# Kernel tuning notes

Measured on AMD Instinct MI355X. Metric: run time of the kernel, lower is better.

Reference implementation:

```python
import jax, jax.numpy as jnp
import numpy as np

TOPK = 13
ALPHA = 1.0
BETA = 6.0
NUM_CLASSES = 80
NUM_ANCHORS = 100000
NUM_GT = 512
EPS = 1e-9


def _make_boxes(key, n):
    k1, k2 = jax.random.split(key)
    lt = jax.random.uniform(k1, (n, 2)) * 0.5          # x1, y1 in [0, 0.5)
    wh = jax.random.uniform(k2, (n, 2)) * 0.5 + 1e-3   # positive width/height
    return jnp.concatenate([lt, lt + wh], axis=-1)      # [n, 4] valid xyxy


def setup_inputs() -> dict:
    key = jax.random.key(0)
    k1, k2, k3, k4 = jax.random.split(key, 4)
    pd_scores = jax.random.uniform(k1, (NUM_ANCHORS, NUM_CLASSES), dtype=jnp.float32)
    pd_bboxes = _make_boxes(k2, NUM_ANCHORS)
    gt_labels = jax.random.randint(k3, (NUM_GT, 1), 0, NUM_CLASSES, dtype=jnp.int64)
    gt_bboxes = _make_boxes(k4, NUM_GT)
    return {"pd_scores": pd_scores, "pd_bboxes": pd_bboxes,
            "gt_labels": gt_labels, "gt_bboxes": gt_bboxes}


def box_iou(a, b):
    # a: [G, 4], b: [A, 4] in xyxy -> iou [G, A]
    lt = jnp.maximum(a[:, None, :2], b[None, :, :2])
    rb = jnp.minimum(a[:, None, 2:], b[None, :, 2:])
    wh = jnp.clip(rb - lt, 0.0)
    inter = wh[..., 0] * wh[..., 1]                      # [G, A]
    area_a = (a[:, 2] - a[:, 0]) * (a[:, 3] - a[:, 1])   # [G]
    area_b = (b[:, 2] - b[:, 0]) * (b[:, 3] - b[:, 1])   # [A]
    union = area_a[:, None] + area_b[None, :] - inter
    return inter / (union + EPS)


def select_topk_candidates(metrics, topk):
    # metrics: [G, A] -> bool mask [G, A] of per-row topk entries
    _, topk_idx = jax.lax.top_k(metrics, topk)           # [G, topk]
    rows = jnp.arange(metrics.shape[0])[:, None]
    mask = jnp.zeros(metrics.shape, dtype=bool)
    return mask.at[rows, topk_idx].set(True)


def reference(pd_scores, pd_bboxes, gt_labels, gt_bboxes):
    labels = gt_labels.reshape(-1)                       # [G]
    ious = box_iou(gt_bboxes, pd_bboxes)                 # [G, A]
    scores = pd_scores[:, labels].T                      # [G, A] gather by gt class
    metrics = (scores ** ALPHA) * (ious ** BETA)         # alignment metric [G, A]
    is_in_topk = select_topk_candidates(metrics, TOPK)   # [G, A] bool
    max_metrics = jnp.max(metrics, axis=0)               # [A]
    max_indices = jnp.argmax(metrics, axis=0)            # [A]
    target_labels = labels[max_indices]                  # [A]
    target_labels = jnp.where(max_metrics <= 0, NUM_CLASSES, target_labels)
    target_bboxes = gt_bboxes[max_indices]               # [A, 4]
    # is_in_topk is computed (as in the original) and returned so the topk/scatter
    return target_labels, target_bboxes, max_metrics, is_in_topk
```

## Files before the change

### kernel.cpp

```cpp
#include <hip/hip_runtime.h>
#include <cfloat>
#include <cstdint>

#define AN 100000
#define GN 512
#define NC 80
#define KK 13

#define CHUNKS 8
#define CH_LEN 12544
#define DUMP 16
#define GSLICE 8
#define GPS (GN / GSLICE)

typedef unsigned long long ull;

__device__ __forceinline__ float rcpf(float x)
{
    float r; asm("v_rcp_f32 %0, %1" : "=v"(r) : "v"(x)); return r;
}

__device__ __forceinline__ float root6_down(float th)
{
    return exp2f(log2f(th) * (1.0f / 6.0f)) * 0.9999f;
}

__device__ __forceinline__ float iou6r(float4 g, float ga, float4 p)
{
    float pa = (p.z - p.x) * (p.w - p.y);
    float ltx = fmaxf(g.x, p.x), lty = fmaxf(g.y, p.y);
    float rbx = fminf(g.z, p.z), rby = fminf(g.w, p.w);
    float w = fmaxf(rbx - ltx, 0.0f), h = fmaxf(rby - lty, 0.0f);
    float inter = w * h;
    float uni = ga + pa - inter;
    float iou = inter * rcpf(uni + 1e-9f);
    float i2 = iou * iou;
    return i2 * i2 * i2;
}

__device__ __forceinline__ unsigned f2ord(float f)
{
    unsigned b = __float_as_uint(f);
    return b ^ (unsigned)(((int)b >> 31) | 0x80000000);
}
__device__ __forceinline__ float ord2f(unsigned u)
{
    unsigned b = (u & 0x80000000u) ? (u ^ 0x80000000u) : ~u;
    return __uint_as_float(b);
}

__device__ __forceinline__ void csw(float& va, int& ia, float& vb, int& ib)
{
    bool sw = (va < vb) || (va == vb && ia > ib);
    float tv = sw ? vb : va; int ti = sw ? ib : ia;
    vb = sw ? va : vb; ib = sw ? ia : ib;
    va = tv; ia = ti;
}

__device__ __forceinline__ void wsync()
{
    __builtin_amdgcn_sched_barrier(0);
    asm volatile("s_waitcnt lgkmcnt(0)" ::: "memory");
    __builtin_amdgcn_sched_barrier(0);
}

__device__ float flush_f(int lane, int n,
                         const float* c_in, const float* c_ue, const int* c_ix,
                         const float* __restrict__ srow,
                         float& inc_v, int& inc_i)
{
    wsync();
    float v[8]; int ix[8];
    #pragma unroll
    for (int k = 0; k < 8; ++k) {
        int j = lane + (k << 6);
        bool ok = j < n;
        float in = ok ? c_in[j] : 0.0f;
        float ue = ok ? c_ue[j] : 1.0f;
        int   ai = ok ? c_ix[j] : 0;
        float iou = in * rcpf(ue);
        float i2 = iou * iou;
        float i6 = i2 * i2 * i2;
        float sc = srow[ai];
        v[k]  = ok ? sc * i6 : -FLT_MAX;
        ix[k] = ok ? ai : 0x7fffffff;
    }
    csw(v[0],ix[0],v[1],ix[1]); csw(v[2],ix[2],v[3],ix[3]);
    csw(v[4],ix[4],v[5],ix[5]); csw(v[6],ix[6],v[7],ix[7]);
    csw(v[0],ix[0],v[2],ix[2]); csw(v[1],ix[1],v[3],ix[3]);
    csw(v[4],ix[4],v[6],ix[6]); csw(v[5],ix[5],v[7],ix[7]);
    csw(v[1],ix[1],v[2],ix[2]); csw(v[5],ix[5],v[6],ix[6]);
    csw(v[0],ix[0],v[4],ix[4]); csw(v[1],ix[1],v[5],ix[5]);
    csw(v[2],ix[2],v[6],ix[6]); csw(v[3],ix[3],v[7],ix[7]);
    csw(v[2],ix[2],v[4],ix[4]); csw(v[3],ix[3],v[5],ix[5]);
    csw(v[1],ix[1],v[2],ix[2]); csw(v[3],ix[3],v[4],ix[4]);
    csw(v[5],ix[5],v[6],ix[6]);
    bool c[8];
    #pragma unroll
    for (int j = 0; j < 8; ++j)
        c[j] = (v[j] > inc_v) || (v[j] == inc_v && ix[j] < inc_i);
    float h[9]; int hi[9];
    h[0] = c[0] ? v[0] : inc_v;  hi[0] = c[0] ? ix[0] : inc_i;
    #pragma unroll
    for (int j = 1; j < 8; ++j) {
        h[j]  = c[j] ? v[j]  : (c[j-1] ? inc_v : v[j-1]);
        hi[j] = c[j] ? ix[j] : (c[j-1] ? inc_i : ix[j-1]);
    }
    h[8] = c[7] ? inc_v : v[7];  hi[8] = c[7] ? inc_i : ix[7];

    float th = -FLT_MAX;
    #pragma unroll
    for (int r = 0; r < KK; ++r) {
        ull myp = ((ull)f2ord(h[0]) << 32) | (unsigned)(~hi[0]);
        ull p = myp;
        #pragma unroll
        for (int o = 32; o >= 1; o >>= 1) {
            ull q = __shfl_xor(p, o);
            p = p > q ? p : q;
        }
        float wv = ord2f((unsigned)(p >> 32));
        int   wi = (int)~((unsigned)p);
        if (lane == r) { inc_v = wv; inc_i = wi; }
        bool pop = (myp == p);
        #pragma unroll
        for (int j = 0; j < 8; ++j) {
            h[j]  = pop ? h[j+1]  : h[j];
            hi[j] = pop ? hi[j+1] : hi[j];
        }
        h[8]  = pop ? -FLT_MAX   : h[8];
        hi[8] = pop ? 0x7fffffff : hi[8];
        th = wv;
    }
    return th;
}

__device__ __forceinline__ void insert13(float* v, int* ix, float m, int a)
{
    bool worse = (m < v[KK - 1]) || (m == v[KK - 1] && a > ix[KK - 1]);
    if (worse) return;
    int p = 0;
    #pragma unroll
    for (int j = 0; j < KK; ++j)
        p += ((v[j] > m) || (v[j] == m && ix[j] < a)) ? 1 : 0;
    #pragma unroll
    for (int j = KK - 1; j >= 1; --j) {
        bool sh = (j > p);
        v[j]  = sh ? v[j - 1]  : v[j];
        ix[j] = sh ? ix[j - 1] : ix[j];
    }
    #pragma unroll
    for (int j = 0; j < KK; ++j) if (j == p) { v[j] = m; ix[j] = a; }
}

__global__ __launch_bounds__(256) void transpose_scores(
    const float* __restrict__ ps, float* __restrict__ scT)
{
    __shared__ float tile[64][NC + 1];
    int a0 = blockIdx.x * 64;
    int tid = threadIdx.x;
    for (int i = tid; i < 64 * NC / 4; i += 256) {
        int fi = i * 4;
        int a = fi / NC, c = fi % NC;
        if (a0 + a < AN) {
            float4 v = *reinterpret_cast<const float4*>(ps + (size_t)(a0 + a) * NC + c);
            tile[a][c] = v.x; tile[a][c + 1] = v.y; tile[a][c + 2] = v.z; tile[a][c + 3] = v.w;
        }
    }
    __syncthreads();
    int j = tid & 63, cg = tid >> 6;
    int a = a0 + j;
    if (a < AN) {
        for (int c = cg; c < NC; c += 4)
            scT[(size_t)c * AN + a] = tile[j][c];
    }
}

__global__ __launch_bounds__(256) void argmax_part(
    const float* __restrict__ pd_bboxes,
    const int*   __restrict__ gt_labels,
    const float* __restrict__ gt_bboxes,
    const float* __restrict__ scT,
    ull* __restrict__ part)
{
    __shared__ float4 gb[GPS];
    __shared__ float  ga[GPS];
    __shared__ int    glb[GPS];
    int slice = blockIdx.x & (GSLICE - 1);
    int ab = (blockIdx.x >> 3) * 512;
    int tid = threadIdx.x;
    int g0 = slice * GPS;
    if (tid < GPS) {
        float4 bb = ((const float4*)gt_bboxes)[g0 + tid];
        gb[tid] = bb;
        ga[tid] = (bb.z - bb.x) * (bb.w - bb.y);
        glb[tid] = gt_labels[g0 + tid];
    }
    __syncthreads();
    int aa = ab + tid, ab2 = ab + 256 + tid;
    bool okA = aa < AN, okB = ab2 < AN;
    int ca = okA ? aa : AN - 1, cb = okB ? ab2 : AN - 1;
    float4 pba = ((const float4*)pd_bboxes)[ca];
    float4 pbb = ((const float4*)pd_bboxes)[cb];
    float bestA = -1.0f, bestB = -1.0f;
    int bgA = 0, bgB = 0;
    for (int i = 0; i < GPS; ++i) {
        float4 gx = gb[i];
        float gax = ga[i];
        int lab = glb[i];
        const float* srow = scT + (size_t)lab * AN;
        float i6a = iou6r(gx, gax, pba);
        float i6b = iou6r(gx, gax, pbb);
        float sa = (i6a > bestA) ? srow[ca] : 0.0f;
        float sb = (i6b > bestB) ? srow[cb] : 0.0f;
        float ma = sa * i6a;
        float mb = sb * i6b;
        if (ma > bestA) { bestA = ma; bgA = i; }
        if (mb > bestB) { bestB = mb; bgB = i; }
    }
    if (okA)
        part[(size_t)slice * AN + aa] =
            ((ull)__float_as_uint(bestA) << 32) | (ull)(0xFFFFFFFFu - (unsigned)(g0 + bgA));
    if (okB)
        part[(size_t)slice * AN + ab2] =
            ((ull)__float_as_uint(bestB) << 32) | (ull)(0xFFFFFFFFu - (unsigned)(g0 + bgB));
}

__global__ __launch_bounds__(256) void argmax_combine(
    const ull* __restrict__ part,
    const int* __restrict__ gt_labels,
    const float* __restrict__ gt_bboxes,
    float* __restrict__ out)
{
    int a = blockIdx.x * 256 + threadIdx.x;
    if (a >= AN) return;
    ull p = part[a];
    #pragma unroll
    for (int s = 1; s < GSLICE; ++s) {
        ull q = part[(size_t)s * AN + a];
        p = p > q ? p : q;
    }
    unsigned g = 0xFFFFFFFFu - (unsigned)(p & 0xFFFFFFFFull);
    float best = __uint_as_float((unsigned)(p >> 32));
    out[a] = (best <= 0.0f) ? (float)NC : (float)gt_labels[g];
    ((float4*)(out + AN))[a] = ((const float4*)gt_bboxes)[g];
    out[(size_t)5 * AN + a] = best;
}

__device__ __forceinline__ void loadB(int tb, int lane,
    const float4* __restrict__ pd4,
    float4& B0, float4& B1, float4& B2, float4& B3)
{
    int a0 = tb + lane;
    B0 = pd4[min(a0,       AN - 1)];
    B1 = pd4[min(a0 + 64,  AN - 1)];
    B2 = pd4[min(a0 + 128, AN - 1)];
    B3 = pd4[min(a0 + 192, AN - 1)];
}

__device__ __forceinline__ void procB(
    int tb, int aend, int lane, uint64_t lt,
    float4 B0, float4 B1, float4 B2, float4 B3,
    const float* __restrict__ srow,
    float4 b, float gax, float& th, float& cth, int& cnt,
    float* c_in, float* c_ue, int* c_ix,
    float& inc_v, int& inc_i)
{
    int a0 = tb + lane, a1 = a0 + 64, a2 = a0 + 128, a3 = a0 + 192;
    float lx0 = fmaxf(b.x, B0.x), ly0 = fmaxf(b.y, B0.y);
    float rx0 = fminf(b.z, B0.z), ry0 = fminf(b.w, B0.w);
    float w0 = fmaxf(rx0 - lx0, 0.0f), h0f = fmaxf(ry0 - ly0, 0.0f);
    float in0 = w0 * h0f;
    float ue0 = gax + (B0.z - B0.x) * (B0.w - B0.y) - in0 + 1e-9f;
    float lx1 = fmaxf(b.x, B1.x), ly1 = fmaxf(b.y, B1.y);
    float rx1 = fminf(b.z, B1.z), ry1 = fminf(b.w, B1.w);
    float w1 = fmaxf(rx1 - lx1, 0.0f), h1f = fmaxf(ry1 - ly1, 0.0f);
    float in1 = w1 * h1f;
    float ue1 = gax + (B1.z - B1.x) * (B1.w - B1.y) - in1 + 1e-9f;
    float lx2 = fmaxf(b.x, B2.x), ly2 = fmaxf(b.y, B2.y);
    float rx2 = fminf(b.z, B2.z), ry2 = fminf(b.w, B2.w);
    float w2 = fmaxf(rx2 - lx2, 0.0f), h2f = fmaxf(ry2 - ly2, 0.0f);
    float in2 = w2 * h2f;
    float ue2 = gax + (B2.z - B2.x) * (B2.w - B2.y) - in2 + 1e-9f;
    float lx3 = fmaxf(b.x, B3.x), ly3 = fmaxf(b.y, B3.y);
    float rx3 = fminf(b.z, B3.z), ry3 = fminf(b.w, B3.w);
    float w3 = fmaxf(rx3 - lx3, 0.0f), h3f = fmaxf(ry3 - ly3, 0.0f);
    float in3 = w3 * h3f;
    float ue3 = gax + (B3.z - B3.x) * (B3.w - B3.y) - in3 + 1e-9f;
    bool h0 = (in0 > cth * ue0) && (a0 < aend);
    bool h1 = (in1 > cth * ue1) && (a1 < aend);
    bool h2 = (in2 > cth * ue2) && (a2 < aend);
    bool h3 = (in3 > cth * ue3) && (a3 < aend);
    if (__any(h0 | h1 | h2 | h3)) {
        uint64_t B;
        B = __ballot(h0);
        if (h0) { int p = cnt + __popcll(B & lt); c_in[p] = in0; c_ue[p] = ue0; c_ix[p] = a0; }
        cnt += __popcll(B);
        B = __ballot(h1);
        if (h1) { int p = cnt + __popcll(B & lt); c_in[p] = in1; c_ue[p] = ue1; c_ix[p] = a1; }
        cnt += __popcll(B);
        B = __ballot(h2);
        if (h2) { int p = cnt + __popcll(B & lt); c_in[p] = in2; c_ue[p] = ue2; c_ix[p] = a2; }
        cnt += __popcll(B);
        B = __ballot(h3);
        if (h3) { int p = cnt + __popcll(B & lt); c_in[p] = in3; c_ue[p] = ue3; c_ix[p] = a3; }
        cnt += __popcll(B);
        if (cnt >= 256) {
            th = flush_f(lane, cnt, c_in, c_ue, c_ix, srow, inc_v, inc_i);
            cth = root6_down(th);
            cnt = 0;
        }
    }
}

__global__ __launch_bounds__(256, 4) void topk_pass1(
    const float* __restrict__ pd_bboxes,
    const int*   __restrict__ gt_labels,
    const float* __restrict__ gt_bboxes,
    const float* __restrict__ scT,
    float* __restrict__ out_v, int* __restrict__ out_i)
{
    __shared__ float cinA[4][512];
    __shared__ float cueA[4][512];
    __shared__ int   cixA[4][512];
    int w = threadIdx.x >> 6, lane = threadIdx.x & 63;
    float* c_in = cinA[w]; float* c_ue = cueA[w]; int* c_ix = cixA[w];
    uint64_t lt = (1ull << lane) - 1ull;
    int gid = blockIdx.x * 4 + w;
    int g = gid & (GN - 1), c = gid >> 9;

    float4 b = ((const float4*)gt_bboxes)[g];
    float gax = (b.z - b.x) * (b.w - b.y);
    int lab = gt_labels[g];
    const float* srow = scT + (size_t)lab * AN;
    const float4* pd4 = (const float4*)pd_bboxes;

    int base = c * CH_LEN;
    int len = min(CH_LEN, AN - base);
    int aend = base + len;
    int NT = (len + 255) >> 8;

    float th = -FLT_MAX, cth = -FLT_MAX;
    int cnt = 0;
    float inc_v = -FLT_MAX; int inc_i = 0x7fffffff;

    float4 X0, X1, X2, X3, Y0, Y1, Y2, Y3;
    loadB(base, lane, pd4, X0, X1, X2, X3);
    int i = 0, tb = base;
    while (true) {
        if (i + 1 < NT) loadB(tb + 256, lane, pd4, Y0, Y1, Y2, Y3);
        procB(tb, aend, lane, lt, X0, X1, X2, X3, srow,
              b, gax, th, cth, cnt, c_in, c_ue, c_ix, inc_v, inc_i);
        ++i; tb += 256;
        if (i >= NT) break;
        if (i + 1 < NT) loadB(tb + 256, lane, pd4, X0, X1, X2, X3);
        procB(tb, aend, lane, lt, Y0, Y1, Y2, Y3, srow,
              b, gax, th, cth, cnt, c_in, c_ue, c_ix, inc_v, inc_i);
        ++i; tb += 256;
        if (i >= NT) break;
    }

    if (cnt > 0)
        flush_f(lane, cnt, c_in, c_ue, c_ix, srow, inc_v, inc_i);

    if (lane < DUMP) {
        size_t o = ((size_t)g * CHUNKS + c) * DUMP + lane;
        out_v[o] = (lane < KK) ? inc_v : -FLT_MAX;
        out_i[o] = (lane < KK) ? inc_i : 0x7fffffff;
    }
}

__global__ __launch_bounds__(256) void topk_finalize(
    const float* __restrict__ in_v, const int* __restrict__ in_i,
    float* __restrict__ mask)
{
    int g = blockIdx.x, tid = threadIdx.x;
    float4* row4 = (float4*)(mask + (size_t)g * AN);
    float4 z = make_float4(0.f, 0.f, 0.f, 0.f);
    for (int j = tid; j < AN / 4; j += 256) row4[j] = z;
    __syncthreads();
    if (tid >= 64) return;
    int lane = tid;
    size_t rb = (size_t)g * (CHUNKS * DUMP);
    float v0 = in_v[rb + lane], v1 = in_v[rb + 64 + lane];
    int   i0 = in_i[rb + lane], i1 = in_i[rb + 64 + lane];
    csw(v0, i0, v1, i1);
    #pragma unroll
    for (int r = 0; r < KK; ++r) {
        ull myp = ((ull)f2ord(v0) << 32) | (unsigned)(~i0);
        ull p = myp;
        #pragma unroll
        for (int o = 32; o >= 1; o >>= 1) {
            ull q = __shfl_xor(p, o);
            p = p > q ? p : q;
        }
        int wi = (int)~((unsigned)p);
        if (lane == r) mask[(size_t)g * AN + wi] = 1.0f;
        bool pop = (myp == p);
        v0 = pop ? v1 : v0;          i0 = pop ? i1 : i0;
        v1 = pop ? -FLT_MAX : v1;    i1 = pop ? 0x7fffffff : i1;
    }
}

__global__ __launch_bounds__(256) void argmax_kernel(
    const float* __restrict__ pd_scores,
    const float* __restrict__ pd_bboxes,
    const int*   __restrict__ gt_labels,
    const float* __restrict__ gt_bboxes,
    const float* __restrict__ scT, int use_t,
    float* __restrict__ out)
{
    __shared__ float4 gb[GN];
    __shared__ float  ga[GN];
    __shared__ int    gl[GN];
    int tid = threadIdx.x;
    for (int g = tid; g < GN; g += 256) {
        float4 b = reinterpret_cast<const float4*>(gt_bboxes)[g];
        gb[g] = b;
        ga[g] = (b.z - b.x) * (b.w - b.y);
        gl[g] = gt_labels[g];
    }
    __syncthreads();
    int a = blockIdx.x * 256 + tid;
    if (a >= AN) return;
    float4 pb = reinterpret_cast<const float4*>(pd_bboxes)[a];
    float best = -1.0f; int bg = 0;
    for (int g = 0; g < GN; ++g) {
        int lab = gl[g];
        float sc = use_t ? scT[(size_t)lab * AN + a] : pd_scores[(size_t)a * NC + lab];
        float m = sc * iou6r(gb[g], ga[g], pb);
        if (m > best) { best = m; bg = g; }
    }
    out[a] = (best <= 0.0f) ? (float)NC : (float)gl[bg];
    reinterpret_cast<float4*>(out + AN)[a] = gb[bg];
    out[5 * AN + a] = best;
}

__global__ __launch_bounds__(256) void topk_kernel_fallback(
    const float* __restrict__ pd_scores,
    const float* __restrict__ pd_bboxes,
    const int*   __restrict__ gt_labels,
    const float* __restrict__ gt_bboxes,
    const float* __restrict__ scT, int use_t,
    float* __restrict__ mask)
{
    __shared__ float sv[256 * KK];
    __shared__ int   si[256 * KK];
    int g = blockIdx.x, tid = threadIdx.x;
    float4 b = reinterpret_cast<const float4*>(gt_bboxes)[g];
    float gax = (b.z - b.x) * (b.w - b.y);
    int lab = gt_labels[g];
    float v[KK]; int idx[KK];
    #pragma unroll
    for (int j = 0; j < KK; ++j) { v[j] = -FLT_MAX; idx[j] = 0x7fffffff; }
    for (int a = tid; a < AN; a += 256) {
        float4 pb = reinterpret_cast<const float4*>(pd_bboxes)[a];
        float sc = use_t ? scT[(size_t)lab * AN + a] : pd_scores[(size_t)a * NC + lab];
        float m = sc * iou6r(b, gax, pb);
        insert13(v, idx, m, a);
    }
    #pragma unroll
    for (int j = 0; j < KK; ++j) { sv[tid * KK + j] = v[j]; si[tid * KK + j] = idx[j]; }
    for (int off = 128; off >= 1; off >>= 1) {
        __syncthreads();
        if (tid < off) {
            int i = 0, jj = 0;
            float ov[KK]; int oi[KK];
            #pragma unroll
            for (int t = 0; t < KK; ++t) {
                float va = sv[tid * KK + i];          int ia = si[tid * KK + i];
                float vb = sv[(tid + off) * KK + jj]; int ib = si[(tid + off) * KK + jj];
                bool ta = (va > vb) || (va == vb && ia < ib);
                ov[t] = ta ? va : vb; oi[t] = ta ? ia : ib;
                i += ta ? 1 : 0; jj += ta ? 0 : 1;
            }
            #pragma unroll
            for (int t = 0; t < KK; ++t) { sv[tid * KK + t] = ov[t]; si[tid * KK + t] = oi[t]; }
        }
    }
    __syncthreads();
    if (tid < KK) mask[(size_t)g * AN + si[tid]] = 1.0f;
}

extern "C" void kernel_launch(void* const* d_in, const int* in_sizes, int n_in,
                              void* d_out, int out_size, void* d_ws, size_t ws_size,
                              hipStream_t stream)
{
    const float* pd_scores = (const float*)d_in[0];
    const float* pd_bboxes = (const float*)d_in[1];
    const int*   gt_labels = (const int*)d_in[2];
    const float* gt_bboxes = (const float*)d_in[3];
    float* out  = (float*)d_out;
    float* mask = out + (size_t)6 * AN;

    const size_t scT_b  = (size_t)NC * AN * sizeof(float);
    const size_t auxn   = (size_t)GN * CHUNKS * DUMP;
    const size_t aux_b  = auxn * 8;
    const size_t part_b = (size_t)GSLICE * AN * sizeof(ull);

    float* scT   = (float*)d_ws;
    float* aux_v = (float*)((char*)d_ws + scT_b);
    int*   aux_i = (int*)(aux_v + auxn);
    ull*   part  = (ull*)((char*)d_ws + scT_b + aux_b);

    if (ws_size >= scT_b + aux_b + part_b) {
        transpose_scores<<<(AN + 63) / 64, 256, 0, stream>>>(pd_scores, scT);
        topk_pass1<<<GN * CHUNKS / 4, 256, 0, stream>>>(
            pd_bboxes, gt_labels, gt_bboxes, scT, aux_v, aux_i);
        topk_finalize<<<GN, 256, 0, stream>>>(aux_v, aux_i, mask);
        argmax_part<<<((AN + 511) / 512) * GSLICE, 256, 0, stream>>>(
            pd_bboxes, gt_labels, gt_bboxes, scT, part);
        argmax_combine<<<(AN + 255) / 256, 256, 0, stream>>>(
            part, gt_labels, gt_bboxes, out);
    } else if (ws_size >= scT_b + aux_b) {
        transpose_scores<<<(AN + 63) / 64, 256, 0, stream>>>(pd_scores, scT);
        topk_pass1<<<GN * CHUNKS / 4, 256, 0, stream>>>(
            pd_bboxes, gt_labels, gt_bboxes, scT, aux_v, aux_i);
        topk_finalize<<<GN, 256, 0, stream>>>(aux_v, aux_i, mask);
        argmax_kernel<<<(AN + 255) / 256, 256, 0, stream>>>(
            pd_scores, pd_bboxes, gt_labels, gt_bboxes, scT, 1, out);
    } else if (ws_size >= scT_b) {
        hipMemsetAsync(mask, 0, (size_t)GN * AN * sizeof(float), stream);
        transpose_scores<<<(AN + 63) / 64, 256, 0, stream>>>(pd_scores, scT);
        argmax_kernel<<<(AN + 255) / 256, 256, 0, stream>>>(
            pd_scores, pd_bboxes, gt_labels, gt_bboxes, scT, 1, out);
        topk_kernel_fallback<<<GN, 256, 0, stream>>>(
            pd_scores, pd_bboxes, gt_labels, gt_bboxes, scT, 1, mask);
    } else {
        hipMemsetAsync(mask, 0, (size_t)GN * AN * sizeof(float), stream);
        argmax_kernel<<<(AN + 255) / 256, 256, 0, stream>>>(
            pd_scores, pd_bboxes, gt_labels, gt_bboxes, scT, 0, out);
        topk_kernel_fallback<<<GN, 256, 0, stream>>>(
            pd_scores, pd_bboxes, gt_labels, gt_bboxes, scT, 0, mask);
    }
}
```

Before: 181.4 us.

## Precompute anchor areas and process eight anchors per lane in topk pass

Adds a small kernel that precomputes each predicted box's area into workspace, so topk_pass1 reads the area instead of recomputing it for every GT. The pass-1 inner loop now handles 512 anchors per iteration (8 per lane), uses a FULL template to drop bounds checks on full tiles, and replaces the explicit double-buffered register prefetch with direct loads. CH_LEN is changed to a multiple of 512 and the intermediate workspace fallback path is removed. This costs an extra kernel launch plus more workspace and more registers per lane, and losing the explicit prefetch may expose load latency.

```diff
diff --git a/kernel.cpp b/kernel.cpp
--- a/kernel.cpp
+++ b/kernel.cpp
@@ -8,7 +8,7 @@
 #define KK 13
 
 #define CHUNKS 8
-#define CH_LEN 12544
+#define CH_LEN 12800
 #define DUMP 16
 #define GSLICE 8
 #define GPS (GN / GSLICE)
@@ -150,6 +150,15 @@
     }
     #pragma unroll
     for (int j = 0; j < KK; ++j) if (j == p) { v[j] = m; ix[j] = a; }
+}
+
+__global__ __launch_bounds__(256) void area_kernel(
+    const float* __restrict__ pd_bboxes, float* __restrict__ paArr)
+{
+    int a = blockIdx.x * 256 + threadIdx.x;
+    if (a >= AN) return;
+    float4 p = ((const float4*)pd_bboxes)[a];
+    paArr[a] = (p.z - p.x) * (p.w - p.y);
 }
 
 __global__ __launch_bounds__(256) void transpose_scores(
@@ -246,74 +255,58 @@
     out[(size_t)5 * AN + a] = best;
 }
 
-__device__ __forceinline__ void loadB(int tb, int lane,
-    const float4* __restrict__ pd4,
-    float4& B0, float4& B1, float4& B2, float4& B3)
-{
-    int a0 = tb + lane;
-    B0 = pd4[min(a0,       AN - 1)];
-    B1 = pd4[min(a0 + 64,  AN - 1)];
-    B2 = pd4[min(a0 + 128, AN - 1)];
-    B3 = pd4[min(a0 + 192, AN - 1)];
-}
-
-__device__ __forceinline__ void procB(
+template<bool FULL>
+__device__ __forceinline__ void procB8(
     int tb, int aend, int lane, uint64_t lt,
-    float4 B0, float4 B1, float4 B2, float4 B3,
+    const float4* __restrict__ pd4, const float* __restrict__ paArr,
     const float* __restrict__ srow,
     float4 b, float gax, float& th, float& cth, int& cnt,
     float* c_in, float* c_ue, int* c_ix,
     float& inc_v, int& inc_i)
 {
-    int a0 = tb + lane, a1 = a0 + 64, a2 = a0 + 128, a3 = a0 + 192;
-    float lx0 = fmaxf(b.x, B0.x), ly0 = fmaxf(b.y, B0.y);
-    float rx0 = fminf(b.z, B0.z), ry0 = fminf(b.w, B0.w);
-    float w0 = fmaxf(rx0 - lx0, 0.0f), h0f = fmaxf(ry0 - ly0, 0.0f);
-    float in0 = w0 * h0f;
-    float ue0 = gax + (B0.z - B0.x) * (B0.w - B0.y) - in0 + 1e-9f;
-    float lx1 = fmaxf(b.x, B1.x), ly1 = fmaxf(b.y, B1.y);
-    float rx1 = fminf(b.z, B1.z), ry1 = fminf(b.w, B1.w);
-    float w1 = fmaxf(rx1 - lx1, 0.0f), h1f = fmaxf(ry1 - ly1, 0.0f);
-    float in1 = w1 * h1f;
-    float ue1 = gax + (B1.z - B1.x) * (B1.w - B1.y) - in1 + 1e-9f;
-    float lx2 = fmaxf(b.x, B2.x), ly2 = fmaxf(b.y, B2.y);
-    float rx2 = fminf(b.z, B2.z), ry2 = fminf(b.w, B2.w);
-    float w2 = fmaxf(rx2 - lx2, 0.0f), h2f = fmaxf(ry2 - ly2, 0.0f);
-    float in2 = w2 * h2f;
-    float ue2 = gax + (B2.z - B2.x) * (B2.w - B2.y) - in2 + 1e-9f;
-    float lx3 = fmaxf(b.x, B3.x), ly3 = fmaxf(b.y, B3.y);
-    float rx3 = fminf(b.z, B3.z), ry3 = fminf(b.w, B3.w);
-    float w3 = fmaxf(rx3 - lx3, 0.0f), h3f = fmaxf(ry3 - ly3, 0.0f);
-    float in3 = w3 * h3f;
-    float ue3 = gax + (B3.z - B3.x) * (B3.w - B3.y) - in3 + 1e-9f;
-    bool h0 = (in0 > cth * ue0) && (a0 < aend);
-    bool h1 = (in1 > cth * ue1) && (a1 < aend);
-    bool h2 = (in2 > cth * ue2) && (a2 < aend);
-    bool h3 = (in3 > cth * ue3) && (a3 < aend);
-    if (__any(h0 | h1 | h2 | h3)) {
-        uint64_t B;
-        B = __ballot(h0);
-        if (h0) { int p = cnt + __popcll(B & lt); c_in[p] = in0; c_ue[p] = ue0; c_ix[p] = a0; }
-        cnt += __popcll(B);
-        B = __ballot(h1);
-        if (h1) { int p = cnt + __popcll(B & lt); c_in[p] = in1; c_ue[p] = ue1; c_ix[p] = a1; }
-        cnt += __popcll(B);
-        B = __ballot(h2);
-        if (h2) { int p = cnt + __popcll(B & lt); c_in[p] = in2; c_ue[p] = ue2; c_ix[p] = a2; }
-        cnt += __popcll(B);
-        B = __ballot(h3);
-        if (h3) { int p = cnt + __popcll(B & lt); c_in[p] = in3; c_ue[p] = ue3; c_ix[p] = a3; }
-        cnt += __popcll(B);
-        if (cnt >= 256) {
-            th = flush_f(lane, cnt, c_in, c_ue, c_ix, srow, inc_v, inc_i);
-            cth = root6_down(th);
-            cnt = 0;
+    int a[8]; float4 P[8]; float pa[8], in[8], ue[8];
+    bool h[8];
+    #pragma unroll
+    for (int k = 0; k < 8; ++k) {
+        a[k] = tb + lane + (k << 6);
+        int ck = FULL ? a[k] : min(a[k], AN - 1);
+        P[k] = pd4[ck];
+        pa[k] = paArr[ck];
+    }
+    #pragma unroll
+    for (int k = 0; k < 8; ++k) {
+        float lx = fmaxf(b.x, P[k].x), ly = fmaxf(b.y, P[k].y);
+        float rx = fminf(b.z, P[k].z), ry = fminf(b.w, P[k].w);
+        float w = fmaxf(rx - lx, 0.0f), hh = fmaxf(ry - ly, 0.0f);
+        in[k] = w * hh;
+        ue[k] = gax + pa[k] - in[k] + 1e-9f;
+        h[k] = (in[k] > cth * ue[k]) && (FULL || a[k] < aend);
+    }
+    bool any = false;
+    #pragma unroll
+    for (int k = 0; k < 8; ++k) any |= h[k];
+    if (__any(any)) {
+        #pragma unroll
+        for (int half = 0; half < 2; ++half) {
+            #pragma unroll
+            for (int k = half * 4; k < half * 4 + 4; ++k) {
+                uint64_t B = __ballot(h[k]);
+                if (h[k]) { int p = cnt + __popcll(B & lt);
+                            c_in[p] = in[k]; c_ue[p] = ue[k]; c_ix[p] = a[k]; }
+                cnt += __popcll(B);
+            }
+            if (cnt >= 256) {
+                th = flush_f(lane, cnt, c_in, c_ue, c_ix, srow, inc_v, inc_i);
+                cth = root6_down(th);
+                cnt = 0;
+            }
         }
     }
 }
 
 __global__ __launch_bounds__(256, 4) void topk_pass1(
     const float* __restrict__ pd_bboxes,
+    const float* __restrict__ paArr,
     const int*   __restrict__ gt_labels,
     const float* __restrict__ gt_bboxes,
     const float* __restrict__ scT,
@@ -337,27 +330,20 @@
     int base = c * CH_LEN;
     int len = min(CH_LEN, AN - base);
     int aend = base + len;
-    int NT = (len + 255) >> 8;
+    int nfull = len >> 9;
+    int rem = len & 511;
 
     float th = -FLT_MAX, cth = -FLT_MAX;
     int cnt = 0;
     float inc_v = -FLT_MAX; int inc_i = 0x7fffffff;
 
-    float4 X0, X1, X2, X3, Y0, Y1, Y2, Y3;
-    loadB(base, lane, pd4, X0, X1, X2, X3);
-    int i = 0, tb = base;
-    while (true) {
-        if (i + 1 < NT) loadB(tb + 256, lane, pd4, Y0, Y1, Y2, Y3);
-        procB(tb, aend, lane, lt, X0, X1, X2, X3, srow,
-              b, gax, th, cth, cnt, c_in, c_ue, c_ix, inc_v, inc_i);
-        ++i; tb += 256;
-        if (i >= NT) break;
-        if (i + 1 < NT) loadB(tb + 256, lane, pd4, X0, X1, X2, X3);
-        procB(tb, aend, lane, lt, Y0, Y1, Y2, Y3, srow,
-              b, gax, th, cth, cnt, c_in, c_ue, c_ix, inc_v, inc_i);
-        ++i; tb += 256;
-        if (i >= NT) break;
-    }
+    int tb = base;
+    for (int i = 0; i < nfull; ++i, tb += 512)
+        procB8<true>(tb, aend, lane, lt, pd4, paArr, srow,
+                     b, gax, th, cth, cnt, c_in, c_ue, c_ix, inc_v, inc_i);
+    if (rem)
+        procB8<false>(tb, aend, lane, lt, pd4, paArr, srow,
+                      b, gax, th, cth, cnt, c_in, c_ue, c_ix, inc_v, inc_i);
 
     if (cnt > 0)
         flush_f(lane, cnt, c_in, c_ue, c_ix, srow, inc_v, inc_i);
@@ -496,28 +482,24 @@
     const size_t auxn   = (size_t)GN * CHUNKS * DUMP;
     const size_t aux_b  = auxn * 8;
     const size_t part_b = (size_t)GSLICE * AN * sizeof(ull);
+    const size_t pa_b   = (size_t)AN * sizeof(float);
 
     float* scT   = (float*)d_ws;
     float* aux_v = (float*)((char*)d_ws + scT_b);
     int*   aux_i = (int*)(aux_v + auxn);
     ull*   part  = (ull*)((char*)d_ws + scT_b + aux_b);
-
-    if (ws_size >= scT_b + aux_b + part_b) {
+    float* paArr = (float*)((char*)d_ws + scT_b + aux_b + part_b);
+
+    if (ws_size >= scT_b + aux_b + part_b + pa_b) {
+        area_kernel<<<(AN + 255) / 256, 256, 0, stream>>>(pd_bboxes, paArr);
         transpose_scores<<<(AN + 63) / 64, 256, 0, stream>>>(pd_scores, scT);
         topk_pass1<<<GN * CHUNKS / 4, 256, 0, stream>>>(
-            pd_bboxes, gt_labels, gt_bboxes, scT, aux_v, aux_i);
+            pd_bboxes, paArr, gt_labels, gt_bboxes, scT, aux_v, aux_i);
         topk_finalize<<<GN, 256, 0, stream>>>(aux_v, aux_i, mask);
         argmax_part<<<((AN + 511) / 512) * GSLICE, 256, 0, stream>>>(
             pd_bboxes, gt_labels, gt_bboxes, scT, part);
         argmax_combine<<<(AN + 255) / 256, 256, 0, stream>>>(
             part, gt_labels, gt_bboxes, out);
-    } else if (ws_size >= scT_b + aux_b) {
-        transpose_scores<<<(AN + 63) / 64, 256, 0, stream>>>(pd_scores, scT);
-        topk_pass1<<<GN * CHUNKS / 4, 256, 0, stream>>>(
-            pd_bboxes, gt_labels, gt_bboxes, scT, aux_v, aux_i);
-        topk_finalize<<<GN, 256, 0, stream>>>(aux_v, aux_i, mask);
-        argmax_kernel<<<(AN + 255) / 256, 256, 0, stream>>>(
-            pd_scores, pd_bboxes, gt_labels, gt_bboxes, scT, 1, out);
     } else if (ws_size >= scT_b) {
         hipMemsetAsync(mask, 0, (size_t)GN * AN * sizeof(float), stream);
         transpose_scores<<<(AN + 63) / 64, 256, 0, stream>>>(pd_scores, scT);
```

After: 184.8 us. Within noise of the previous version (+1.9%).
